# Kernel tuning notes

Hardware: AMD Instinct MI355X
Metric: run time of the kernel (lower is better)

Reference implementation:

```python
import jax, jax.numpy as jnp
import numpy as np

D_MODEL = 1024
NUM_HEADS = 16
D_K = D_MODEL // NUM_HEADS
BATCH = 4
SEQ = 2048


def setup_inputs() -> dict:
    key = jax.random.key(0)
    ks = jax.random.split(key, 16)
    s = 0.02
    return {
        "query": jax.random.normal(ks[0], (BATCH, SEQ, D_MODEL), jnp.float32),
        "key": jax.random.normal(ks[1], (BATCH, SEQ, D_MODEL), jnp.float32),
        "value": jax.random.normal(ks[2], (BATCH, SEQ, D_MODEL), jnp.float32),
        "Wq": jax.random.normal(ks[3], (D_MODEL, D_MODEL), jnp.float32) * s,
        "bq": jnp.zeros((D_MODEL,), jnp.float32),
        "Wk": jax.random.normal(ks[4], (D_MODEL, D_MODEL), jnp.float32) * s,
        "bk": jnp.zeros((D_MODEL,), jnp.float32),
        "Wv": jax.random.normal(ks[5], (D_MODEL, D_MODEL), jnp.float32) * s,
        "bv": jnp.zeros((D_MODEL,), jnp.float32),
        "Wo": jax.random.normal(ks[6], (D_MODEL, D_MODEL), jnp.float32) * s,
        "bo": jnp.zeros((D_MODEL,), jnp.float32),
        "gamma": jnp.ones((D_MODEL,), jnp.float32),
        "beta": jnp.zeros((D_MODEL,), jnp.float32),
    }


def _layer_norm(x, gamma, beta, eps=1e-5):
    mu = jnp.mean(x, axis=-1, keepdims=True)
    var = jnp.var(x, axis=-1, keepdims=True)
    return (x - mu) * jax.lax.rsqrt(var + eps) * gamma + beta


def reference(query, key, value, Wq, bq, Wk, bk, Wv, bv, Wo, bo, gamma, beta):
    B, S, _ = query.shape
    residual = query
    # projections -> [B, H, S, d_k]
    Q = (query @ Wq + bq).reshape(B, S, NUM_HEADS, D_K).transpose(0, 2, 1, 3)
    K = (key @ Wk + bk).reshape(B, -1, NUM_HEADS, D_K).transpose(0, 2, 1, 3)
    V = (value @ Wv + bv).reshape(B, -1, NUM_HEADS, D_K).transpose(0, 2, 1, 3)
    scale = 1.0 / jnp.sqrt(jnp.asarray(D_K, query.dtype))
    scores = jnp.einsum("bhqd,bhkd->bhqk", Q, K) * scale  # [B,H,S,S]
    attn = jax.nn.softmax(scores, axis=-1)
    ctx = jnp.einsum("bhqk,bhkd->bhqd", attn, V)
    ctx = ctx.transpose(0, 2, 1, 3).reshape(B, S, D_MODEL)
    out = ctx @ Wo + bo
    return _layer_norm(residual + out, gamma, beta)
```

## Files before the change

### kernel.cpp

```cpp
#include <hip/hip_runtime.h>

#define D_MODEL 1024
#define NUM_HEADS 16
#define DK 64
#define BATCH 4
#define SEQ 2048
#define MTOT (BATCH*SEQ)

typedef __attribute__((ext_vector_type(8))) short short8;
typedef __attribute__((ext_vector_type(4))) float f32x4;
typedef __attribute__((ext_vector_type(4))) unsigned int u32x4;

__device__ __forceinline__ unsigned short f2bf(float f) {
    union { float f; unsigned u; } v; v.f = f;
    unsigned r = v.u + 0x7FFFu + ((v.u >> 16) & 1u);
    return (unsigned short)(r >> 16);
}

__device__ __forceinline__ unsigned cvtpk(float lo, float hi) {
    unsigned r;
    asm("v_cvt_pk_bf16_f32 %0, %1, %2" : "=v"(r) : "v"(lo), "v"(hi));
    return r;
}

__device__ __forceinline__ void gload16(const unsigned short* g, unsigned short* l) {
    __builtin_amdgcn_global_load_lds(
        (const __attribute__((address_space(1))) unsigned int*)g,
        (__attribute__((address_space(3))) unsigned int*)l, 16, 0, 0);
}

__global__ __launch_bounds__(256) void mha_wtrans4(
    const float* __restrict__ W0, const float* __restrict__ W1,
    const float* __restrict__ W2, const float* __restrict__ W3,
    unsigned short* __restrict__ T0, unsigned short* __restrict__ T1,
    unsigned short* __restrict__ T2, unsigned short* __restrict__ T3) {
    __shared__ float tile[64][65];
    int z = blockIdx.z;
    const float* W = z == 0 ? W0 : z == 1 ? W1 : z == 2 ? W2 : W3;
    unsigned short* WT = z == 0 ? T0 : z == 1 ? T1 : z == 2 ? T2 : T3;
    int n0 = blockIdx.x * 64, k0 = blockIdx.y * 64;
    int tx = threadIdx.x & 63, ty = threadIdx.x >> 6;
#pragma unroll
    for (int i = 0; i < 16; ++i)
        tile[ty + i * 4][tx] = W[(size_t)(k0 + ty + i * 4) * D_MODEL + n0 + tx];
    __syncthreads();
#pragma unroll
    for (int i = 0; i < 16; ++i)
        WT[(size_t)(n0 + ty + i * 4) * D_MODEL + k0 + tx] = f2bf(tile[tx][ty + i * 4]);
}

__global__ __launch_bounds__(256) void mha_cvt3(
    const float* __restrict__ i0, const float* __restrict__ i1, const float* __restrict__ i2,
    unsigned short* __restrict__ o0, unsigned short* __restrict__ o1, unsigned short* __restrict__ o2) {
    int y = blockIdx.y;
    const float* in = y == 0 ? i0 : y == 1 ? i1 : i2;
    unsigned short* out = y == 0 ? o0 : y == 1 ? o1 : o2;
    int i = blockIdx.x * 256 + threadIdx.x;
    float4 v = reinterpret_cast<const float4*>(in)[i];
    ushort4 o;
    o.x = f2bf(v.x); o.y = f2bf(v.y); o.z = f2bf(v.z); o.w = f2bf(v.w);
    reinterpret_cast<ushort4*>(out)[i] = o;
}

__device__ __forceinline__ void gemm_stage(const unsigned short* Ag, const unsigned short* Bg,
                                           unsigned short* Al, unsigned short* Bl,
                                           int wid, int rsub, int c8, int kk,
                                           int brow, int bcol) {
#pragma unroll
    for (int q = 0; q < 4; ++q) {
        int i = wid * 4 + q;
        int row = i * 8 + rsub;
        int gcol = kk + ((c8 ^ (row & 7)) << 3);
        gload16(Ag + (size_t)(brow + row) * D_MODEL + gcol, Al + i * 512);
        gload16(Bg + (size_t)(bcol + row) * D_MODEL + gcol, Bl + i * 512);
    }
}

__device__ __forceinline__ void gemm_compute(const unsigned short* Al, const unsigned short* Bl,
                                             f32x4 (&acc)[4][4],
                                             int wr, int wc, int l15, int lg, int l7) {
    short8 af[4][2], bf[4][2];
#pragma unroll
    for (int mi = 0; mi < 4; ++mi)
#pragma unroll
        for (int ks = 0; ks < 2; ++ks)
            af[mi][ks] = *reinterpret_cast<const short8*>(
                &Al[(wr * 64 + mi * 16 + l15) * 64 + (((ks * 4 + lg) ^ l7) << 3)]);
#pragma unroll
    for (int ni = 0; ni < 4; ++ni)
#pragma unroll
        for (int ks = 0; ks < 2; ++ks)
            bf[ni][ks] = *reinterpret_cast<const short8*>(
                &Bl[(wc * 64 + ni * 16 + l15) * 64 + (((ks * 4 + lg) ^ l7) << 3)]);
#pragma unroll
    for (int mi = 0; mi < 4; ++mi)
#pragma unroll
        for (int ni = 0; ni < 4; ++ni)
#pragma unroll
            for (int ks = 0; ks < 2; ++ks)
                acc[mi][ni] = __builtin_amdgcn_mfma_f32_16x16x32_bf16(
                    af[mi][ks], bf[ni][ks], acc[mi][ni], 0, 0, 0);
}

__global__ __launch_bounds__(256) void mha_gemm_qkv(
    const unsigned short* __restrict__ Aq, const unsigned short* __restrict__ Ak,
    const unsigned short* __restrict__ Av,
    const unsigned short* __restrict__ Wq, const unsigned short* __restrict__ Wk,
    const unsigned short* __restrict__ Wv,
    const float* __restrict__ bq, const float* __restrict__ bk, const float* __restrict__ bv,
    unsigned short* __restrict__ Qb, unsigned short* __restrict__ Kb,
    unsigned short* __restrict__ VT, float qscale) {
    __shared__ unsigned short SM[32768];
    unsigned short* A0 = SM;
    unsigned short* B0 = SM + 8192;
    unsigned short* A1 = SM + 16384;
    unsigned short* B1 = SM + 24576;

    int z = blockIdx.z;
    const unsigned short* A = z == 0 ? Aq : z == 1 ? Ak : Av;
    const unsigned short* WT = z == 0 ? Wq : z == 1 ? Wk : Wv;
    const float* bias = z == 0 ? bq : z == 1 ? bk : bv;

    int wid = threadIdx.x >> 6;
    int lane = threadIdx.x & 63;
    int wr = wid >> 1, wc = wid & 1;
    int brow = blockIdx.x * 128;
    int bcol = blockIdx.y * 128;
    int l15 = lane & 15, lg = lane >> 4;
    int c8 = lane & 7, rsub = lane >> 3;
    int l7 = l15 & 7;

    f32x4 acc[4][4] = {};
    gemm_stage(A, WT, A0, B0, wid, rsub, c8, 0, brow, bcol);
    __syncthreads();
    for (int kk = 0; kk < D_MODEL; kk += 128) {
        gemm_stage(A, WT, A1, B1, wid, rsub, c8, kk + 64, brow, bcol);
        gemm_compute(A0, B0, acc, wr, wc, l15, lg, l7);
        __syncthreads();
        if (kk + 128 < D_MODEL)
            gemm_stage(A, WT, A0, B0, wid, rsub, c8, kk + 128, brow, bcol);
        gemm_compute(A1, B1, acc, wr, wc, l15, lg, l7);
        __syncthreads();
    }

    if (z < 2) {
        unsigned short* outb = z == 0 ? Qb : Kb;
        float scale = z == 0 ? qscale : 1.0f;
#pragma unroll
        for (int ni = 0; ni < 4; ++ni) {
            int col = bcol + wc * 64 + ni * 16 + l15;
            float bv2 = bias[col];
#pragma unroll
            for (int mi = 0; mi < 4; ++mi)
#pragma unroll
                for (int j = 0; j < 4; ++j) {
                    int row = brow + wr * 64 + mi * 16 + lg * 4 + j;
                    outb[(size_t)row * D_MODEL + col] = f2bf((acc[mi][ni][j] + bv2) * scale);
                }
        }
    } else {
        unsigned short* T = SM;
#pragma unroll
        for (int ni = 0; ni < 4; ++ni) {
            int c = wc * 64 + ni * 16 + l15;
            float bv2 = bias[bcol + c];
#pragma unroll
            for (int mi = 0; mi < 4; ++mi)
#pragma unroll
                for (int j = 0; j < 4; ++j) {
                    int r = wr * 64 + mi * 16 + lg * 4 + j;
                    T[c * 136 + r] = f2bf(acc[mi][ni][j] + bv2);
                }
        }
        __syncthreads();
        int c = threadIdx.x >> 1;
        int rh = (threadIdx.x & 1) * 64;
        int gcol = bcol + c;
        int h = gcol >> 6, d = gcol & 63;
        int b = brow >> 11, s0 = brow & (SEQ - 1);
        unsigned short* dst = VT + ((size_t)((b * 16 + h) * 64 + d)) * SEQ + s0 + rh;
        const unsigned short* src = &T[c * 136 + rh];
#pragma unroll
        for (int i = 0; i < 8; ++i)
            *reinterpret_cast<short8*>(dst + i * 8) =
                *reinterpret_cast<const short8*>(src + i * 8);
    }
}

__global__ __launch_bounds__(256) void mha_gemm_o(const unsigned short* __restrict__ A,
                                                  const unsigned short* __restrict__ WT,
                                                  const float* __restrict__ bias,
                                                  const float* __restrict__ residual,
                                                  float* __restrict__ outf) {
    __shared__ unsigned short SM[32768];
    unsigned short* A0 = SM;
    unsigned short* B0 = SM + 8192;
    unsigned short* A1 = SM + 16384;
    unsigned short* B1 = SM + 24576;

    int wid = threadIdx.x >> 6;
    int lane = threadIdx.x & 63;
    int wr = wid >> 1, wc = wid & 1;
    int brow = blockIdx.x * 128;
    int bcol = blockIdx.y * 128;
    int l15 = lane & 15, lg = lane >> 4;
    int c8 = lane & 7, rsub = lane >> 3;
    int l7 = l15 & 7;

    f32x4 acc[4][4] = {};
    gemm_stage(A, WT, A0, B0, wid, rsub, c8, 0, brow, bcol);
    __syncthreads();
    for (int kk = 0; kk < D_MODEL; kk += 128) {
        gemm_stage(A, WT, A1, B1, wid, rsub, c8, kk + 64, brow, bcol);
        gemm_compute(A0, B0, acc, wr, wc, l15, lg, l7);
        __syncthreads();
        if (kk + 128 < D_MODEL)
            gemm_stage(A, WT, A0, B0, wid, rsub, c8, kk + 128, brow, bcol);
        gemm_compute(A1, B1, acc, wr, wc, l15, lg, l7);
        __syncthreads();
    }
#pragma unroll
    for (int ni = 0; ni < 4; ++ni) {
        int col = bcol + wc * 64 + ni * 16 + l15;
        float bv2 = bias[col];
#pragma unroll
        for (int mi = 0; mi < 4; ++mi)
#pragma unroll
            for (int j = 0; j < 4; ++j) {
                int row = brow + wr * 64 + mi * 16 + lg * 4 + j;
                outf[(size_t)row * D_MODEL + col] =
                    acc[mi][ni][j] + bv2 + residual[(size_t)row * D_MODEL + col];
            }
    }
}

__device__ __forceinline__ void attn_tile(const unsigned short* Kd,
                                          const unsigned short* Vd,
                                          const short8 aq[2][2],
                                          f32x4 (&acc)[2][4],
                                          float (&lsum)[2],
                                          int l15, int lg, int l7) {
    f32x4 z[2][4];
#pragma unroll
    for (int t = 0; t < 4; ++t) {
        int krow = (t * 16 + l15) * 64;
        short8 kf0 = *reinterpret_cast<const short8*>(&Kd[krow + ((lg ^ l7) << 3)]);
        short8 kf1 = *reinterpret_cast<const short8*>(&Kd[krow + (((4 + lg) ^ l7) << 3)]);
#pragma unroll
        for (int m = 0; m < 2; ++m) {
            f32x4 zz = {};
            zz = __builtin_amdgcn_mfma_f32_16x16x32_bf16(kf0, aq[m][0], zz, 0, 0, 0);
            zz = __builtin_amdgcn_mfma_f32_16x16x32_bf16(kf1, aq[m][1], zz, 0, 0, 0);
            z[m][t] = zz;
        }
    }
#pragma unroll
    for (int m = 0; m < 2; ++m)
#pragma unroll
        for (int t = 0; t < 4; ++t)
#pragma unroll
            for (int j = 0; j < 4; ++j) {
                float p = __builtin_amdgcn_exp2f(z[m][t][j]);
                z[m][t][j] = p;
                lsum[m] += p;
            }
    short8 pf[2][2];
#pragma unroll
    for (int m = 0; m < 2; ++m)
#pragma unroll
        for (int ks = 0; ks < 2; ++ks) {
            union { u32x4 u; short8 s; } cv;
            cv.u = (u32x4){cvtpk(z[m][2 * ks][0], z[m][2 * ks][1]),
                           cvtpk(z[m][2 * ks][2], z[m][2 * ks][3]),
                           cvtpk(z[m][2 * ks + 1][0], z[m][2 * ks + 1][1]),
                           cvtpk(z[m][2 * ks + 1][2], z[m][2 * ks + 1][3])};
            pf[m][ks] = cv.s;
        }
#pragma unroll
    for (int dt = 0; dt < 4; ++dt) {
        int vrow = (dt * 16 + l15) * 64;
        short8 vf0 = *reinterpret_cast<const short8*>(&Vd[vrow + ((lg ^ l7) << 3)]);
        short8 vf1 = *reinterpret_cast<const short8*>(&Vd[vrow + (((4 + lg) ^ l7) << 3)]);
#pragma unroll
        for (int m = 0; m < 2; ++m) {
            acc[m][dt] = __builtin_amdgcn_mfma_f32_16x16x32_bf16(vf0, pf[m][0], acc[m][dt], 0, 0, 0);
            acc[m][dt] = __builtin_amdgcn_mfma_f32_16x16x32_bf16(vf1, pf[m][1], acc[m][dt], 0, 0, 0);
        }
    }
}

__global__ __launch_bounds__(256, 4) void mha_attn(const unsigned short* __restrict__ Q,
                                                   const unsigned short* __restrict__ K,
                                                   const unsigned short* __restrict__ VT,
                                                   unsigned short* __restrict__ ctx) {
    __shared__ unsigned short K0[64 * 64], V0[64 * 64];
    __shared__ unsigned short K1[64 * 64], V1[64 * 64];

    int lane = threadIdx.x & 63;
    int w = threadIdx.x >> 6;
    int l15 = lane & 15, lg = lane >> 4;
    int l7 = l15 & 7;
    int c8 = lane & 7, rsub = lane >> 3;

    int id = blockIdx.x + gridDim.x * blockIdx.y;
    int nid = (id & 7) * 128 + (id >> 3);
    int bx = nid & 15;
    int bh = nid >> 4;
    int b = bh >> 4, h = bh & 15;
    int q0 = bx * 128 + w * 32;

    short8 aq[2][2];
    {
        const unsigned short* Qp = Q + (size_t)(b * SEQ + q0) * D_MODEL + h * DK;
#pragma unroll
        for (int m = 0; m < 2; ++m)
#pragma unroll
            for (int ks = 0; ks < 2; ++ks)
                aq[m][ks] = *reinterpret_cast<const short8*>(
                    Qp + (size_t)(m * 16 + l15) * D_MODEL + ks * 32 + lg * 8);
    }

    f32x4 acc[2][4] = {};
    float lsum[2] = {};

    const unsigned short* Kbh = K + (size_t)(b * SEQ) * D_MODEL + h * DK;
    const unsigned short* VTbh = VT + (size_t)bh * DK * SEQ;

    int i0 = w * 2, i1 = w * 2 + 1;
    int row0 = i0 * 8 + rsub, row1 = i1 * 8 + rsub;
    int sw0 = (c8 ^ (row0 & 7)) << 3, sw1 = (c8 ^ (row1 & 7)) << 3;
    int sr0 = (row0 & 32) | ((row0 & 12) << 1) | ((row0 & 16) >> 2) | (row0 & 3);
    int sr1 = (row1 & 32) | ((row1 & 12) << 1) | ((row1 & 16) >> 2) | (row1 & 3);

#define STAGE(Kd, Vd, kb)                                                        \
    do {                                                                         \
        gload16(Kbh + (size_t)((kb) + sr0) * D_MODEL + sw0, (Kd) + i0 * 512);    \
        gload16(Kbh + (size_t)((kb) + sr1) * D_MODEL + sw1, (Kd) + i1 * 512);    \
        gload16(VTbh + (size_t)row0 * SEQ + (kb) + sw0, (Vd) + i0 * 512);        \
        gload16(VTbh + (size_t)row1 * SEQ + (kb) + sw1, (Vd) + i1 * 512);        \
    } while (0)

    STAGE(K0, V0, 0);
    __syncthreads();

    for (int kb = 0; kb < SEQ; kb += 128) {
        STAGE(K1, V1, kb + 64);
        attn_tile(K0, V0, aq, acc, lsum, l15, lg, l7);
        __syncthreads();
        if (kb + 128 < SEQ) STAGE(K0, V0, kb + 128);
        attn_tile(K1, V1, aq, acc, lsum, l15, lg, l7);
        __syncthreads();
    }
#undef STAGE

#pragma unroll
    for (int m = 0; m < 2; ++m) {
        float l = lsum[m];
        l += __shfl_xor(l, 16);
        l += __shfl_xor(l, 32);
        float rl = 1.0f / l;
        int q = q0 + m * 16 + l15;
        unsigned short* cp = ctx + (size_t)(b * SEQ + q) * D_MODEL + h * DK + lg * 4;
#pragma unroll
        for (int dt = 0; dt < 4; ++dt) {
            ushort4 o;
            o.x = f2bf(acc[m][dt][0] * rl);
            o.y = f2bf(acc[m][dt][1] * rl);
            o.z = f2bf(acc[m][dt][2] * rl);
            o.w = f2bf(acc[m][dt][3] * rl);
            *reinterpret_cast<ushort4*>(cp + dt * 16) = o;
        }
    }
}

__global__ __launch_bounds__(256) void mha_ln(const float* __restrict__ X,
                                              const float* __restrict__ gamma,
                                              const float* __restrict__ beta,
                                              float* __restrict__ out) {
    int row = blockIdx.x;
    int t = threadIdx.x;
    const float* x = X + (size_t)row * D_MODEL;
    float4 v = reinterpret_cast<const float4*>(x)[t];
    float s = v.x + v.y + v.z + v.w;
    float s2 = v.x * v.x + v.y * v.y + v.z * v.z + v.w * v.w;
#pragma unroll
    for (int off = 1; off < 64; off <<= 1) {
        s += __shfl_xor(s, off);
        s2 += __shfl_xor(s2, off);
    }
    __shared__ float ws[8];
    int wid = t >> 6;
    if ((t & 63) == 0) { ws[wid] = s; ws[4 + wid] = s2; }
    __syncthreads();
    s = ws[0] + ws[1] + ws[2] + ws[3];
    s2 = ws[4] + ws[5] + ws[6] + ws[7];
    float mu = s * (1.f / D_MODEL);
    float var = s2 * (1.f / D_MODEL) - mu * mu;
    float rstd = rsqrtf(var + 1e-5f);
    float4 gv = reinterpret_cast<const float4*>(gamma)[t];
    float4 bv = reinterpret_cast<const float4*>(beta)[t];
    float4 o;
    o.x = (v.x - mu) * rstd * gv.x + bv.x;
    o.y = (v.y - mu) * rstd * gv.y + bv.y;
    o.z = (v.z - mu) * rstd * gv.z + bv.z;
    o.w = (v.w - mu) * rstd * gv.w + bv.w;
    reinterpret_cast<float4*>(out + (size_t)row * D_MODEL)[t] = o;
}

extern "C" void kernel_launch(void* const* d_in, const int* in_sizes, int n_in,
                              void* d_out, int out_size, void* d_ws, size_t ws_size,
                              hipStream_t stream) {
    const float* query = (const float*)d_in[0];
    const float* key   = (const float*)d_in[1];
    const float* value = (const float*)d_in[2];
    const float* Wq = (const float*)d_in[3];
    const float* bq = (const float*)d_in[4];
    const float* Wk = (const float*)d_in[5];
    const float* bk = (const float*)d_in[6];
    const float* Wv = (const float*)d_in[7];
    const float* bv = (const float*)d_in[8];
    const float* Wo = (const float*)d_in[9];
    const float* bo = (const float*)d_in[10];
    const float* gamma = (const float*)d_in[11];
    const float* beta  = (const float*)d_in[12];

    char* ws = (char*)d_ws;
    const size_t MB = 1u << 20;
    unsigned short* WTq = (unsigned short*)(ws + 0 * MB);
    unsigned short* WTk = (unsigned short*)(ws + 2 * MB);
    unsigned short* WTv = (unsigned short*)(ws + 4 * MB);
    unsigned short* WTo = (unsigned short*)(ws + 6 * MB);
    unsigned short* Aq  = (unsigned short*)(ws + 8 * MB);
    unsigned short* Ak  = (unsigned short*)(ws + 24 * MB);
    unsigned short* Av  = (unsigned short*)(ws + 40 * MB);
    unsigned short* Qb  = (unsigned short*)(ws + 56 * MB);
    unsigned short* Kb  = (unsigned short*)(ws + 72 * MB);
    unsigned short* VT  = (unsigned short*)(ws + 88 * MB);
    unsigned short* ctx = (unsigned short*)(ws + 92 * MB);
    float* tmp          = (float*)(ws + 24 * MB);

    const float C1 = 0.180336880f;

    dim3 b256(256);
    mha_wtrans4<<<dim3(16, 16, 4), b256, 0, stream>>>(Wq, Wk, Wv, Wo, WTq, WTk, WTv, WTo);

    int nblk = (MTOT * D_MODEL / 4) / 256;
    mha_cvt3<<<dim3(nblk, 3), b256, 0, stream>>>(query, key, value, Aq, Ak, Av);

    mha_gemm_qkv<<<dim3(MTOT / 128, D_MODEL / 128, 3), b256, 0, stream>>>(
        Aq, Ak, Av, WTq, WTk, WTv, bq, bk, bv, Qb, Kb, VT, C1);

    mha_attn<<<dim3(SEQ / 128, BATCH * NUM_HEADS), b256, 0, stream>>>(Qb, Kb, VT, ctx);

    mha_gemm_o<<<dim3(MTOT / 128, D_MODEL / 128), b256, 0, stream>>>(ctx, WTo, bo, query, tmp);

    mha_ln<<<dim3(MTOT), b256, 0, stream>>>(tmp, gamma, beta, (float*)d_out);
}
```

Baseline: 200.2 us.

## Fuse fp32→bf16 input conversion into QKV GEMM; load V fragments directly in attention

The standalone conversion kernel is removed. The QKV GEMM now reads fp32 activations straight from global memory into registers and packs them to bf16 A-fragments, so only the weight tile is staged through LDS. This removes a full write and reread of three bf16 activation copies, but A is no longer shared through LDS, so each wave re-reads its fp32 rows and issues more global traffic. In attention, V fragments are loaded directly from global into registers instead of LDS, the row-sum is kept as vector partials, s_setprio hints are added around the MFMA sections, and the launch-bounds occupancy hint is dropped.

```diff
diff --git a/kernel.cpp b/kernel.cpp
--- a/kernel.cpp
+++ b/kernel.cpp
@@ -49,75 +49,31 @@
         WT[(size_t)(n0 + ty + i * 4) * D_MODEL + k0 + tx] = f2bf(tile[tx][ty + i * 4]);
 }
 
-__global__ __launch_bounds__(256) void mha_cvt3(
-    const float* __restrict__ i0, const float* __restrict__ i1, const float* __restrict__ i2,
-    unsigned short* __restrict__ o0, unsigned short* __restrict__ o1, unsigned short* __restrict__ o2) {
-    int y = blockIdx.y;
-    const float* in = y == 0 ? i0 : y == 1 ? i1 : i2;
-    unsigned short* out = y == 0 ? o0 : y == 1 ? o1 : o2;
-    int i = blockIdx.x * 256 + threadIdx.x;
-    float4 v = reinterpret_cast<const float4*>(in)[i];
-    ushort4 o;
-    o.x = f2bf(v.x); o.y = f2bf(v.y); o.z = f2bf(v.z); o.w = f2bf(v.w);
-    reinterpret_cast<ushort4*>(out)[i] = o;
-}
-
-__device__ __forceinline__ void gemm_stage(const unsigned short* Ag, const unsigned short* Bg,
-                                           unsigned short* Al, unsigned short* Bl,
-                                           int wid, int rsub, int c8, int kk,
-                                           int brow, int bcol) {
+__device__ __forceinline__ void stageB(const unsigned short* Bg, unsigned short* Bl,
+                                       int wid, int rsub, int c8, int kk, int bcol) {
 #pragma unroll
     for (int q = 0; q < 4; ++q) {
         int i = wid * 4 + q;
         int row = i * 8 + rsub;
         int gcol = kk + ((c8 ^ (row & 7)) << 3);
-        gload16(Ag + (size_t)(brow + row) * D_MODEL + gcol, Al + i * 512);
         gload16(Bg + (size_t)(bcol + row) * D_MODEL + gcol, Bl + i * 512);
     }
 }
 
-__device__ __forceinline__ void gemm_compute(const unsigned short* Al, const unsigned short* Bl,
-                                             f32x4 (&acc)[4][4],
-                                             int wr, int wc, int l15, int lg, int l7) {
-    short8 af[4][2], bf[4][2];
-#pragma unroll
-    for (int mi = 0; mi < 4; ++mi)
-#pragma unroll
-        for (int ks = 0; ks < 2; ++ks)
-            af[mi][ks] = *reinterpret_cast<const short8*>(
-                &Al[(wr * 64 + mi * 16 + l15) * 64 + (((ks * 4 + lg) ^ l7) << 3)]);
-#pragma unroll
-    for (int ni = 0; ni < 4; ++ni)
-#pragma unroll
-        for (int ks = 0; ks < 2; ++ks)
-            bf[ni][ks] = *reinterpret_cast<const short8*>(
-                &Bl[(wc * 64 + ni * 16 + l15) * 64 + (((ks * 4 + lg) ^ l7) << 3)]);
-#pragma unroll
-    for (int mi = 0; mi < 4; ++mi)
-#pragma unroll
-        for (int ni = 0; ni < 4; ++ni)
-#pragma unroll
-            for (int ks = 0; ks < 2; ++ks)
-                acc[mi][ni] = __builtin_amdgcn_mfma_f32_16x16x32_bf16(
-                    af[mi][ks], bf[ni][ks], acc[mi][ni], 0, 0, 0);
-}
-
-__global__ __launch_bounds__(256) void mha_gemm_qkv(
-    const unsigned short* __restrict__ Aq, const unsigned short* __restrict__ Ak,
-    const unsigned short* __restrict__ Av,
+__global__ __launch_bounds__(256) void mha_gemm_qkvf(
+    const float* __restrict__ Aq, const float* __restrict__ Ak,
+    const float* __restrict__ Av,
     const unsigned short* __restrict__ Wq, const unsigned short* __restrict__ Wk,
     const unsigned short* __restrict__ Wv,
     const float* __restrict__ bq, const float* __restrict__ bk, const float* __restrict__ bv,
     unsigned short* __restrict__ Qb, unsigned short* __restrict__ Kb,
     unsigned short* __restrict__ VT, float qscale) {
-    __shared__ unsigned short SM[32768];
-    unsigned short* A0 = SM;
-    unsigned short* B0 = SM + 8192;
-    unsigned short* A1 = SM + 16384;
-    unsigned short* B1 = SM + 24576;
+    __shared__ unsigned short SM[17408];
+    unsigned short* B0 = SM;
+    unsigned short* B1 = SM + 8192;
 
     int z = blockIdx.z;
-    const unsigned short* A = z == 0 ? Aq : z == 1 ? Ak : Av;
+    const float* A = z == 0 ? Aq : z == 1 ? Ak : Av;
     const unsigned short* WT = z == 0 ? Wq : z == 1 ? Wk : Wv;
     const float* bias = z == 0 ? bq : z == 1 ? bk : bv;
 
@@ -130,18 +86,61 @@
     int c8 = lane & 7, rsub = lane >> 3;
     int l7 = l15 & 7;
 
+    const float* Ab = A + (size_t)(brow + wr * 64 + l15) * D_MODEL + lg * 8;
+
     f32x4 acc[4][4] = {};
-    gemm_stage(A, WT, A0, B0, wid, rsub, c8, 0, brow, bcol);
+    stageB(WT, B0, wid, rsub, c8, 0, bcol);
     __syncthreads();
+
+#define AFRAGS(af, kk)                                                          \
+    do {                                                                        \
+        _Pragma("unroll")                                                       \
+        for (int mi = 0; mi < 4; ++mi) {                                        \
+            _Pragma("unroll")                                                   \
+            for (int ks = 0; ks < 2; ++ks) {                                    \
+                const float* ap = Ab + (size_t)(mi * 16) * D_MODEL + (kk) + ks * 32; \
+                float4 a0 = *reinterpret_cast<const float4*>(ap);               \
+                float4 a1 = *reinterpret_cast<const float4*>(ap + 4);           \
+                union { u32x4 u; short8 s; } cv;                                \
+                cv.u = (u32x4){cvtpk(a0.x, a0.y), cvtpk(a0.z, a0.w),            \
+                               cvtpk(a1.x, a1.y), cvtpk(a1.z, a1.w)};           \
+                af[mi][ks] = cv.s;                                              \
+            }                                                                   \
+        }                                                                       \
+    } while (0)
+
+#define BCOMP(Bl, af)                                                           \
+    do {                                                                        \
+        short8 bf[4][2];                                                        \
+        _Pragma("unroll")                                                       \
+        for (int ni = 0; ni < 4; ++ni)                                          \
+            _Pragma("unroll")                                                   \
+            for (int ks = 0; ks < 2; ++ks)                                      \
+                bf[ni][ks] = *reinterpret_cast<const short8*>(                  \
+                    &Bl[(wc * 64 + ni * 16 + l15) * 64 + (((ks * 4 + lg) ^ l7) << 3)]); \
+        _Pragma("unroll")                                                       \
+        for (int mi = 0; mi < 4; ++mi)                                          \
+            _Pragma("unroll")                                                   \
+            for (int ni = 0; ni < 4; ++ni)                                      \
+                _Pragma("unroll")                                               \
+                for (int ks = 0; ks < 2; ++ks)                                  \
+                    acc[mi][ni] = __builtin_amdgcn_mfma_f32_16x16x32_bf16(      \
+                        af[mi][ks], bf[ni][ks], acc[mi][ni], 0, 0, 0);          \
+    } while (0)
+
     for (int kk = 0; kk < D_MODEL; kk += 128) {
-        gemm_stage(A, WT, A1, B1, wid, rsub, c8, kk + 64, brow, bcol);
-        gemm_compute(A0, B0, acc, wr, wc, l15, lg, l7);
-        __syncthreads();
-        if (kk + 128 < D_MODEL)
-            gemm_stage(A, WT, A0, B0, wid, rsub, c8, kk + 128, brow, bcol);
-        gemm_compute(A1, B1, acc, wr, wc, l15, lg, l7);
-        __syncthreads();
-    }
+        short8 afA[4][2], afB[4][2];
+        AFRAGS(afA, kk);
+        stageB(WT, B1, wid, rsub, c8, kk + 64, bcol);
+        BCOMP(B0, afA);
+        __syncthreads();
+        AFRAGS(afB, kk + 64);
+        if (kk + 128 < D_MODEL) stageB(WT, B0, wid, rsub, c8, kk + 128, bcol);
+        BCOMP(B1, afB);
+        __syncthreads();
+    }
+#undef AFRAGS
+#undef BCOMP
 
     if (z < 2) {
         unsigned short* outb = z == 0 ? Qb : Kb;
@@ -185,6 +184,46 @@
             *reinterpret_cast<short8*>(dst + i * 8) =
                 *reinterpret_cast<const short8*>(src + i * 8);
     }
+}
+
+__device__ __forceinline__ void gemm_stage(const unsigned short* Ag, const unsigned short* Bg,
+                                           unsigned short* Al, unsigned short* Bl,
+                                           int wid, int rsub, int c8, int kk,
+                                           int brow, int bcol) {
+#pragma unroll
+    for (int q = 0; q < 4; ++q) {
+        int i = wid * 4 + q;
+        int row = i * 8 + rsub;
+        int gcol = kk + ((c8 ^ (row & 7)) << 3);
+        gload16(Ag + (size_t)(brow + row) * D_MODEL + gcol, Al + i * 512);
+        gload16(Bg + (size_t)(bcol + row) * D_MODEL + gcol, Bl + i * 512);
+    }
+}
+
+__device__ __forceinline__ void gemm_compute(const unsigned short* Al, const unsigned short* Bl,
+                                             f32x4 (&acc)[4][4],
+                                             int wr, int wc, int l15, int lg, int l7) {
+    short8 af[4][2], bf[4][2];
+#pragma unroll
+    for (int mi = 0; mi < 4; ++mi)
+#pragma unroll
+        for (int ks = 0; ks < 2; ++ks)
+            af[mi][ks] = *reinterpret_cast<const short8*>(
+                &Al[(wr * 64 + mi * 16 + l15) * 64 + (((ks * 4 + lg) ^ l7) << 3)]);
+#pragma unroll
+    for (int ni = 0; ni < 4; ++ni)
+#pragma unroll
+        for (int ks = 0; ks < 2; ++ks)
+            bf[ni][ks] = *reinterpret_cast<const short8*>(
+                &Bl[(wc * 64 + ni * 16 + l15) * 64 + (((ks * 4 + lg) ^ l7) << 3)]);
+#pragma unroll
+    for (int mi = 0; mi < 4; ++mi)
+#pragma unroll
+        for (int ni = 0; ni < 4; ++ni)
+#pragma unroll
+            for (int ks = 0; ks < 2; ++ks)
+                acc[mi][ni] = __builtin_amdgcn_mfma_f32_16x16x32_bf16(
+                    af[mi][ks], bf[ni][ks], acc[mi][ni], 0, 0, 0);
 }
 
 __global__ __launch_bounds__(256) void mha_gemm_o(const unsigned short* __restrict__ A,
@@ -235,12 +274,13 @@
 }
 
 __device__ __forceinline__ void attn_tile(const unsigned short* Kd,
-                                          const unsigned short* Vd,
+                                          const short8 (&vf)[4][2],
                                           const short8 aq[2][2],
                                           f32x4 (&acc)[2][4],
-                                          float (&lsum)[2],
+                                          f32x4 (&lsv)[2],
                                           int l15, int lg, int l7) {
     f32x4 z[2][4];
+    __builtin_amdgcn_s_setprio(1);
 #pragma unroll
     for (int t = 0; t < 4; ++t) {
         int krow = (t * 16 + l15) * 64;
@@ -254,16 +294,19 @@
             z[m][t] = zz;
         }
     }
-#pragma unroll
-    for (int m = 0; m < 2; ++m)
-#pragma unroll
-        for (int t = 0; t < 4; ++t)
-#pragma unroll
-            for (int j = 0; j < 4; ++j) {
-                float p = __builtin_amdgcn_exp2f(z[m][t][j]);
-                z[m][t][j] = p;
-                lsum[m] += p;
-            }
+    __builtin_amdgcn_s_setprio(0);
+#pragma unroll
+    for (int m = 0; m < 2; ++m) {
+#pragma unroll
+        for (int t = 0; t < 4; ++t) {
+#pragma unroll
+            for (int j = 0; j < 4; ++j)
+                z[m][t][j] = __builtin_amdgcn_exp2f(z[m][t][j]);
+        }
+        f32x4 s01 = z[m][0] + z[m][1];
+        f32x4 s23 = z[m][2] + z[m][3];
+        lsv[m] += (s01 + s23);
+    }
     short8 pf[2][2];
 #pragma unroll
     for (int m = 0; m < 2; ++m)
@@ -276,25 +319,22 @@
                            cvtpk(z[m][2 * ks + 1][2], z[m][2 * ks + 1][3])};
             pf[m][ks] = cv.s;
         }
-#pragma unroll
-    for (int dt = 0; dt < 4; ++dt) {
-        int vrow = (dt * 16 + l15) * 64;
-        short8 vf0 = *reinterpret_cast<const short8*>(&Vd[vrow + ((lg ^ l7) << 3)]);
-        short8 vf1 = *reinterpret_cast<const short8*>(&Vd[vrow + (((4 + lg) ^ l7) << 3)]);
+    __builtin_amdgcn_s_setprio(1);
+#pragma unroll
+    for (int dt = 0; dt < 4; ++dt)
 #pragma unroll
         for (int m = 0; m < 2; ++m) {
-            acc[m][dt] = __builtin_amdgcn_mfma_f32_16x16x32_bf16(vf0, pf[m][0], acc[m][dt], 0, 0, 0);
-            acc[m][dt] = __builtin_amdgcn_mfma_f32_16x16x32_bf16(vf1, pf[m][1], acc[m][dt], 0, 0, 0);
-        }
-    }
-}
-
-__global__ __launch_bounds__(256, 4) void mha_attn(const unsigned short* __restrict__ Q,
-                                                   const unsigned short* __restrict__ K,
-                                                   const unsigned short* __restrict__ VT,
-                                                   unsigned short* __restrict__ ctx) {
-    __shared__ unsigned short K0[64 * 64], V0[64 * 64];
-    __shared__ unsigned short K1[64 * 64], V1[64 * 64];
+            acc[m][dt] = __builtin_amdgcn_mfma_f32_16x16x32_bf16(vf[dt][0], pf[m][0], acc[m][dt], 0, 0, 0);
+            acc[m][dt] = __builtin_amdgcn_mfma_f32_16x16x32_bf16(vf[dt][1], pf[m][1], acc[m][dt], 0, 0, 0);
+        }
+    __builtin_amdgcn_s_setprio(0);
+}
+
+__global__ __launch_bounds__(256) void mha_attn(const unsigned short* __restrict__ Q,
+                                                const unsigned short* __restrict__ K,
+                                                const unsigned short* __restrict__ VT,
+                                                unsigned short* __restrict__ ctx) {
+    __shared__ unsigned short K0[64 * 64], K1[64 * 64];
 
     int lane = threadIdx.x & 63;
     int w = threadIdx.x >> 6;
@@ -321,7 +361,7 @@
     }
 
     f32x4 acc[2][4] = {};
-    float lsum[2] = {};
+    f32x4 lsv[2] = {};
 
     const unsigned short* Kbh = K + (size_t)(b * SEQ) * D_MODEL + h * DK;
     const unsigned short* VTbh = VT + (size_t)bh * DK * SEQ;
@@ -332,30 +372,42 @@
     int sr0 = (row0 & 32) | ((row0 & 12) << 1) | ((row0 & 16) >> 2) | (row0 & 3);
     int sr1 = (row1 & 32) | ((row1 & 12) << 1) | ((row1 & 16) >> 2) | (row1 & 3);
 
-#define STAGE(Kd, Vd, kb)                                                        \
+#define STAGE_K(Kd, kb)                                                          \
     do {                                                                         \
         gload16(Kbh + (size_t)((kb) + sr0) * D_MODEL + sw0, (Kd) + i0 * 512);    \
         gload16(Kbh + (size_t)((kb) + sr1) * D_MODEL + sw1, (Kd) + i1 * 512);    \
-        gload16(VTbh + (size_t)row0 * SEQ + (kb) + sw0, (Vd) + i0 * 512);        \
-        gload16(VTbh + (size_t)row1 * SEQ + (kb) + sw1, (Vd) + i1 * 512);        \
     } while (0)
 
-    STAGE(K0, V0, 0);
+#define VLOAD(vf, kb)                                                            \
+    do {                                                                         \
+        _Pragma("unroll")                                                        \
+        for (int dt = 0; dt < 4; ++dt)                                           \
+            _Pragma("unroll")                                                    \
+            for (int ks = 0; ks < 2; ++ks)                                       \
+                vf[dt][ks] = *reinterpret_cast<const short8*>(                   \
+                    VTbh + (size_t)(dt * 16 + l15) * SEQ + (kb) + ks * 32 + lg * 8); \
+    } while (0)
+
+    STAGE_K(K0, 0);
     __syncthreads();
 
     for (int kb = 0; kb < SEQ; kb += 128) {
-        STAGE(K1, V1, kb + 64);
-        attn_tile(K0, V0, aq, acc, lsum, l15, lg, l7);
-        __syncthreads();
-        if (kb + 128 < SEQ) STAGE(K0, V0, kb + 128);
-        attn_tile(K1, V1, aq, acc, lsum, l15, lg, l7);
-        __syncthreads();
-    }
-#undef STAGE
+        short8 vfA[4][2], vfB[4][2];
+        VLOAD(vfA, kb);
+        STAGE_K(K1, kb + 64);
+        attn_tile(K0, vfA, aq, acc, lsv, l15, lg, l7);
+        __syncthreads();
+        VLOAD(vfB, kb + 64);
+        if (kb + 128 < SEQ) STAGE_K(K0, kb + 128);
+        attn_tile(K1, vfB, aq, acc, lsv, l15, lg, l7);
+        __syncthreads();
+    }
+#undef STAGE_K
+#undef VLOAD
 
 #pragma unroll
     for (int m = 0; m < 2; ++m) {
-        float l = lsum[m];
+        float l = (lsv[m][0] + lsv[m][1]) + (lsv[m][2] + lsv[m][3]);
         l += __shfl_xor(l, 16);
         l += __shfl_xor(l, 32);
         float rl = 1.0f / l;
@@ -430,25 +482,19 @@
     unsigned short* WTk = (unsigned short*)(ws + 2 * MB);
     unsigned short* WTv = (unsigned short*)(ws + 4 * MB);
     unsigned short* WTo = (unsigned short*)(ws + 6 * MB);
-    unsigned short* Aq  = (unsigned short*)(ws + 8 * MB);
-    unsigned short* Ak  = (unsigned short*)(ws + 24 * MB);
-    unsigned short* Av  = (unsigned short*)(ws + 40 * MB);
-    unsigned short* Qb  = (unsigned short*)(ws + 56 * MB);
-    unsigned short* Kb  = (unsigned short*)(ws + 72 * MB);
-    unsigned short* VT  = (unsigned short*)(ws + 88 * MB);
-    unsigned short* ctx = (unsigned short*)(ws + 92 * MB);
-    float* tmp          = (float*)(ws + 24 * MB);
+    unsigned short* Qb  = (unsigned short*)(ws + 8 * MB);
+    unsigned short* Kb  = (unsigned short*)(ws + 25 * MB);
+    unsigned short* VT  = (unsigned short*)(ws + 42 * MB);
+    unsigned short* ctx = (unsigned short*)(ws + 59 * MB);
+    float* tmp          = (float*)(ws + 8 * MB);
 
     const float C1 = 0.180336880f;
 
     dim3 b256(256);
     mha_wtrans4<<<dim3(16, 16, 4), b256, 0, stream>>>(Wq, Wk, Wv, Wo, WTq, WTk, WTv, WTo);
 
-    int nblk = (MTOT * D_MODEL / 4) / 256;
-    mha_cvt3<<<dim3(nblk, 3), b256, 0, stream>>>(query, key, value, Aq, Ak, Av);
-
-    mha_gemm_qkv<<<dim3(MTOT / 128, D_MODEL / 128, 3), b256, 0, stream>>>(
-        Aq, Ak, Av, WTq, WTk, WTv, bq, bk, bv, Qb, Kb, VT, C1);
+    mha_gemm_qkvf<<<dim3(MTOT / 128, D_MODEL / 128, 3), b256, 0, stream>>>(
+        query, key, value, WTq, WTk, WTv, bq, bk, bv, Qb, Kb, VT, C1);
 
     mha_attn<<<dim3(SEQ / 128, BATCH * NUM_HEADS), b256, 0, stream>>>(Qb, Kb, VT, ctx);
 
```

Measured after the change: 369.4 us. 1.85x slower.

## Fuse fp32-to-bf16 input conversion into QKV projection GEMM staging

Applied to the files above, without the earlier changes.

Drops the separate conversion kernel that wrote bf16 copies of query, key and value. The QKV GEMM now loads fp32 A tiles into registers, packs them to bf16 with v_cvt_pk_bf16_f32, and writes them to LDS, software-pipelined around the MFMA compute. This removes one launch and a full write-then-read round trip of three 8192x1024 activation tensors. In exchange the GEMM reads twice the A bytes per tile (redundantly across the 8 column blocks) and uses more registers, which may lower occupancy.

```diff
diff --git a/kernel.cpp b/kernel.cpp
--- a/kernel.cpp
+++ b/kernel.cpp
@@ -49,29 +49,13 @@
         WT[(size_t)(n0 + ty + i * 4) * D_MODEL + k0 + tx] = f2bf(tile[tx][ty + i * 4]);
 }
 
-__global__ __launch_bounds__(256) void mha_cvt3(
-    const float* __restrict__ i0, const float* __restrict__ i1, const float* __restrict__ i2,
-    unsigned short* __restrict__ o0, unsigned short* __restrict__ o1, unsigned short* __restrict__ o2) {
-    int y = blockIdx.y;
-    const float* in = y == 0 ? i0 : y == 1 ? i1 : i2;
-    unsigned short* out = y == 0 ? o0 : y == 1 ? o1 : o2;
-    int i = blockIdx.x * 256 + threadIdx.x;
-    float4 v = reinterpret_cast<const float4*>(in)[i];
-    ushort4 o;
-    o.x = f2bf(v.x); o.y = f2bf(v.y); o.z = f2bf(v.z); o.w = f2bf(v.w);
-    reinterpret_cast<ushort4*>(out)[i] = o;
-}
-
-__device__ __forceinline__ void gemm_stage(const unsigned short* Ag, const unsigned short* Bg,
-                                           unsigned short* Al, unsigned short* Bl,
-                                           int wid, int rsub, int c8, int kk,
-                                           int brow, int bcol) {
+__device__ __forceinline__ void stageB(const unsigned short* Bg, unsigned short* Bl,
+                                       int wid, int rsub, int c8, int kk, int bcol) {
 #pragma unroll
     for (int q = 0; q < 4; ++q) {
         int i = wid * 4 + q;
         int row = i * 8 + rsub;
         int gcol = kk + ((c8 ^ (row & 7)) << 3);
-        gload16(Ag + (size_t)(brow + row) * D_MODEL + gcol, Al + i * 512);
         gload16(Bg + (size_t)(bcol + row) * D_MODEL + gcol, Bl + i * 512);
     }
 }
@@ -102,9 +86,9 @@
                     af[mi][ks], bf[ni][ks], acc[mi][ni], 0, 0, 0);
 }
 
-__global__ __launch_bounds__(256) void mha_gemm_qkv(
-    const unsigned short* __restrict__ Aq, const unsigned short* __restrict__ Ak,
-    const unsigned short* __restrict__ Av,
+__global__ __launch_bounds__(256) void mha_gemm_qkvc(
+    const float* __restrict__ Aqf, const float* __restrict__ Akf,
+    const float* __restrict__ Avf,
     const unsigned short* __restrict__ Wq, const unsigned short* __restrict__ Wk,
     const unsigned short* __restrict__ Wv,
     const float* __restrict__ bq, const float* __restrict__ bk, const float* __restrict__ bv,
@@ -117,7 +101,7 @@
     unsigned short* B1 = SM + 24576;
 
     int z = blockIdx.z;
-    const unsigned short* A = z == 0 ? Aq : z == 1 ? Ak : Av;
+    const float* A = z == 0 ? Aqf : z == 1 ? Akf : Avf;
     const unsigned short* WT = z == 0 ? Wq : z == 1 ? Wk : Wv;
     const float* bias = z == 0 ? bq : z == 1 ? bk : bv;
 
@@ -130,18 +114,65 @@
     int c8 = lane & 7, rsub = lane >> 3;
     int l7 = l15 & 7;
 
+    int arow[4], acol[4];
+#pragma unroll
+    for (int q = 0; q < 4; ++q) {
+        int i = wid * 4 + q;
+        int row = i * 8 + rsub;
+        arow[q] = row;
+        acol[q] = (c8 ^ (row & 7)) << 3;
+    }
+
+#define ALOAD(rA, kk)                                                            \
+    do {                                                                         \
+        _Pragma("unroll")                                                        \
+        for (int q = 0; q < 4; ++q) {                                            \
+            const float* ap = A + (size_t)(brow + arow[q]) * D_MODEL + (kk) + acol[q]; \
+            rA[q][0] = *reinterpret_cast<const float4*>(ap);                     \
+            rA[q][1] = *reinterpret_cast<const float4*>(ap + 4);                 \
+        }                                                                        \
+    } while (0)
+
+#define AWRITE(rA, Al)                                                           \
+    do {                                                                         \
+        _Pragma("unroll")                                                        \
+        for (int q = 0; q < 4; ++q) {                                            \
+            int i = wid * 4 + q;                                                 \
+            u32x4 u = (u32x4){cvtpk(rA[q][0].x, rA[q][0].y),                     \
+                              cvtpk(rA[q][0].z, rA[q][0].w),                     \
+                              cvtpk(rA[q][1].x, rA[q][1].y),                     \
+                              cvtpk(rA[q][1].z, rA[q][1].w)};                    \
+            *reinterpret_cast<u32x4*>(Al + i * 512 + rsub * 64 + c8 * 8) = u;    \
+        }                                                                        \
+    } while (0)
+
     f32x4 acc[4][4] = {};
-    gemm_stage(A, WT, A0, B0, wid, rsub, c8, 0, brow, bcol);
-    __syncthreads();
+    {
+        float4 r0[4][2];
+        ALOAD(r0, 0);
+        stageB(WT, B0, wid, rsub, c8, 0, bcol);
+        AWRITE(r0, A0);
+        __syncthreads();
+    }
     for (int kk = 0; kk < D_MODEL; kk += 128) {
-        gemm_stage(A, WT, A1, B1, wid, rsub, c8, kk + 64, brow, bcol);
+        float4 rB[4][2];
+        ALOAD(rB, kk + 64);
+        stageB(WT, B1, wid, rsub, c8, kk + 64, bcol);
         gemm_compute(A0, B0, acc, wr, wc, l15, lg, l7);
-        __syncthreads();
-        if (kk + 128 < D_MODEL)
-            gemm_stage(A, WT, A0, B0, wid, rsub, c8, kk + 128, brow, bcol);
+        AWRITE(rB, A1);
+        __syncthreads();
+        bool more = (kk + 128) < D_MODEL;
+        float4 rC[4][2];
+        if (more) {
+            ALOAD(rC, kk + 128);
+            stageB(WT, B0, wid, rsub, c8, kk + 128, bcol);
+        }
         gemm_compute(A1, B1, acc, wr, wc, l15, lg, l7);
-        __syncthreads();
-    }
+        if (more) AWRITE(rC, A0);
+        __syncthreads();
+    }
+#undef ALOAD
+#undef AWRITE
 
     if (z < 2) {
         unsigned short* outb = z == 0 ? Qb : Kb;
@@ -184,6 +215,20 @@
         for (int i = 0; i < 8; ++i)
             *reinterpret_cast<short8*>(dst + i * 8) =
                 *reinterpret_cast<const short8*>(src + i * 8);
+    }
+}
+
+__device__ __forceinline__ void gemm_stage(const unsigned short* Ag, const unsigned short* Bg,
+                                           unsigned short* Al, unsigned short* Bl,
+                                           int wid, int rsub, int c8, int kk,
+                                           int brow, int bcol) {
+#pragma unroll
+    for (int q = 0; q < 4; ++q) {
+        int i = wid * 4 + q;
+        int row = i * 8 + rsub;
+        int gcol = kk + ((c8 ^ (row & 7)) << 3);
+        gload16(Ag + (size_t)(brow + row) * D_MODEL + gcol, Al + i * 512);
+        gload16(Bg + (size_t)(bcol + row) * D_MODEL + gcol, Bl + i * 512);
     }
 }
 
@@ -430,25 +475,19 @@
     unsigned short* WTk = (unsigned short*)(ws + 2 * MB);
     unsigned short* WTv = (unsigned short*)(ws + 4 * MB);
     unsigned short* WTo = (unsigned short*)(ws + 6 * MB);
-    unsigned short* Aq  = (unsigned short*)(ws + 8 * MB);
-    unsigned short* Ak  = (unsigned short*)(ws + 24 * MB);
-    unsigned short* Av  = (unsigned short*)(ws + 40 * MB);
-    unsigned short* Qb  = (unsigned short*)(ws + 56 * MB);
-    unsigned short* Kb  = (unsigned short*)(ws + 72 * MB);
-    unsigned short* VT  = (unsigned short*)(ws + 88 * MB);
-    unsigned short* ctx = (unsigned short*)(ws + 92 * MB);
-    float* tmp          = (float*)(ws + 24 * MB);
+    unsigned short* Qb  = (unsigned short*)(ws + 8 * MB);
+    unsigned short* Kb  = (unsigned short*)(ws + 25 * MB);
+    unsigned short* VT  = (unsigned short*)(ws + 42 * MB);
+    unsigned short* ctx = (unsigned short*)(ws + 59 * MB);
+    float* tmp          = (float*)(ws + 8 * MB);
 
     const float C1 = 0.180336880f;
 
     dim3 b256(256);
     mha_wtrans4<<<dim3(16, 16, 4), b256, 0, stream>>>(Wq, Wk, Wv, Wo, WTq, WTk, WTv, WTo);
 
-    int nblk = (MTOT * D_MODEL / 4) / 256;
-    mha_cvt3<<<dim3(nblk, 3), b256, 0, stream>>>(query, key, value, Aq, Ak, Av);
-
-    mha_gemm_qkv<<<dim3(MTOT / 128, D_MODEL / 128, 3), b256, 0, stream>>>(
-        Aq, Ak, Av, WTq, WTk, WTv, bq, bk, bv, Qb, Kb, VT, C1);
+    mha_gemm_qkvc<<<dim3(MTOT / 128, D_MODEL / 128, 3), b256, 0, stream>>>(
+        query, key, value, WTq, WTk, WTv, bq, bk, bv, Qb, Kb, VT, C1);
 
     mha_attn<<<dim3(SEQ / 128, BATCH * NUM_HEADS), b256, 0, stream>>>(Qb, Kb, VT, ctx);
 
```

New measurement: 198.0 us. Within noise of the previous version (-1.1%).
